# Kernel tuning notes

Hardware: AMD Instinct MI355X
Metric: run time of the kernel (lower is better)

## Reference

```python
import jax, jax.numpy as jnp
import numpy as np

B, C, H, W = 16, 256, 64, 64
WS, NH = 8, 4
HD = C // NH
EPS = 1e-5


def setup_inputs() -> dict:
    key = jax.random.key(0)
    ks = jax.random.split(key, 32)
    s = 0.02
    d = {}
    d['x'] = jax.random.normal(ks[0], (B, C, H, W), jnp.float32)
    d['conv1_w'] = jax.random.normal(ks[1], (C, C, 1, 1), jnp.float32) * s
    d['conv1_b'] = jnp.zeros((C,), jnp.float32)
    d['bn1_g'] = jnp.ones((C,), jnp.float32)
    d['bn1_b'] = jnp.zeros((C,), jnp.float32)
    d['bn1_m'] = jax.random.normal(ks[2], (C,), jnp.float32) * 0.1
    d['bn1_v'] = jax.random.uniform(ks[3], (C,), jnp.float32, 0.5, 1.5)
    d['dw_w'] = jax.random.normal(ks[4], (C, 1, 3, 3), jnp.float32) * s
    d['dw_b'] = jnp.zeros((C,), jnp.float32)
    d['bn2_g'] = jnp.ones((C,), jnp.float32)
    d['bn2_b'] = jnp.zeros((C,), jnp.float32)
    d['bn2_m'] = jax.random.normal(ks[5], (C,), jnp.float32) * 0.1
    d['bn2_v'] = jax.random.uniform(ks[6], (C,), jnp.float32, 0.5, 1.5)
    d['conv3_w'] = jax.random.normal(ks[7], (C, C, 1, 1), jnp.float32) * s
    d['conv3_b'] = jnp.zeros((C,), jnp.float32)
    d['ln1_g'] = jnp.ones((C,), jnp.float32)
    d['ln1_b'] = jnp.zeros((C,), jnp.float32)
    d['qkv_w'] = jax.random.normal(ks[8], (3 * C, C), jnp.float32) * s
    d['qkv_b'] = jnp.zeros((3 * C,), jnp.float32)
    d['proj_w'] = jax.random.normal(ks[9], (C, C), jnp.float32) * s
    d['proj_b'] = jnp.zeros((C,), jnp.float32)
    d['ln2_g'] = jnp.ones((C,), jnp.float32)
    d['ln2_b'] = jnp.zeros((C,), jnp.float32)
    d['mlp_w1'] = jax.random.normal(ks[10], (4 * C, C), jnp.float32) * s
    d['mlp_b1'] = jnp.zeros((4 * C,), jnp.float32)
    d['mlp_w2'] = jax.random.normal(ks[11], (C, 4 * C), jnp.float32) * s
    d['mlp_b2'] = jnp.zeros((C,), jnp.float32)
    return d


def _bn(x, g, b, m, v):
    # eval-mode BatchNorm2d over channel dim of NCHW
    inv = g / jnp.sqrt(v + EPS)
    return x * inv[None, :, None, None] + (b - m * inv)[None, :, None, None]


def _ln(x, g, b):
    mu = x.mean(-1, keepdims=True)
    var = ((x - mu) ** 2).mean(-1, keepdims=True)
    return (x - mu) / jnp.sqrt(var + EPS) * g + b


def reference(x, conv1_w, conv1_b, bn1_g, bn1_b, bn1_m, bn1_v, dw_w, dw_b,
              bn2_g, bn2_b, bn2_m, bn2_v, conv3_w, conv3_b, ln1_g, ln1_b,
              qkv_w, qkv_b, proj_w, proj_b, ln2_g, ln2_b,
              mlp_w1, mlp_b1, mlp_w2, mlp_b2):
    # H,W divisible by WS -> no padding
    # conv path: 1x1 -> BN -> dw3x3 -> BN -> 1x1, residual
    h = jnp.einsum('bchw,oc->bohw', x, conv1_w[:, :, 0, 0]) + conv1_b[None, :, None, None]
    h = _bn(h, bn1_g, bn1_b, bn1_m, bn1_v)
    h = jax.lax.conv_general_dilated(h, dw_w, (1, 1), 'SAME',
                                     feature_group_count=C,
                                     dimension_numbers=('NCHW', 'OIHW', 'NCHW'))
    h = h + dw_b[None, :, None, None]
    h = _bn(h, bn2_g, bn2_b, bn2_m, bn2_v)
    h = jnp.einsum('bchw,oc->bohw', h, conv3_w[:, :, 0, 0]) + conv3_b[None, :, None, None]
    x = x + h

    attn_res = x
    # window partition: (B,C,H,W) -> (B*nWin, WS*WS, C)
    w = x.reshape(B, C, H // WS, WS, W // WS, WS)
    w = w.transpose(0, 2, 4, 3, 5, 1).reshape(-1, WS * WS, C)
    w = _ln(w, ln1_g, ln1_b)

    B_, N, _ = w.shape
    qkv = w @ qkv_w.T + qkv_b                      # (B_, N, 3C)
    qkv = qkv.reshape(B_, N, 3, NH, HD).transpose(2, 0, 3, 1, 4)
    q, k, v = qkv[0], qkv[1], qkv[2]               # (B_, NH, N, HD)
    attn = jax.nn.softmax(jnp.einsum('bhnd,bhmd->bhnm', q, k) * (HD ** -0.5), axis=-1)
    o = jnp.einsum('bhnm,bhmd->bhnd', attn, v)
    o = o.transpose(0, 2, 1, 3).reshape(B_, N, C)
    o = o @ proj_w.T + proj_b
    # window reverse
    o = o.reshape(B, H // WS, W // WS, WS, WS, C)
    o = o.transpose(0, 5, 1, 3, 2, 4).reshape(B, C, H, W)
    x = o + attn_res

    ffn_res = x
    t = x.transpose(0, 2, 3, 1)                    # (B,H,W,C)
    t = _ln(t, ln2_g, ln2_b)
    t = jax.nn.gelu(t @ mlp_w1.T + mlp_b1, approximate=False) @ mlp_w2.T + mlp_b2
    x = ffn_res + t.transpose(0, 3, 1, 2)
    return x
```

## Files before the change

kernel.cpp:

```cpp
#include <hip/hip_runtime.h>
#include <hip/hip_bf16.h>

#define EPS 1e-5f

typedef __attribute__((ext_vector_type(8))) short bf16x8;
typedef __attribute__((ext_vector_type(4))) float f32x4;
typedef __attribute__((ext_vector_type(4))) short s16x4;

__device__ __forceinline__ float b2f(ushort u) {
    union { uint i; float f; } v; v.i = ((uint)u) << 16; return v.f;
}
__device__ __forceinline__ ushort f2b(float f) {
    uint x = __float_as_uint(f);
    return (ushort)((x + 0x7fffu + ((x >> 16) & 1u)) >> 16);
}

#define ASYNC16(dst_lds, src_g) \
    __builtin_amdgcn_global_load_lds((const __attribute__((address_space(1))) void*)(src_g), \
                                     (__attribute__((address_space(3))) void*)(dst_lds), 16, 0, 0)

__global__ void k_fold_conv1(const float* __restrict__ w, const float* __restrict__ cb,
                             const float* __restrict__ g, const float* __restrict__ be,
                             const float* __restrict__ mn, const float* __restrict__ vr,
                             ushort* __restrict__ Wf, float* __restrict__ bf) {
    int i = blockIdx.x * 256 + threadIdx.x;
    int o = i >> 8;
    float inv = g[o] * rsqrtf(vr[o] + EPS);
    Wf[i] = f2b(w[i] * inv);
    if ((i & 255) == 0) bf[o] = cb[o] * inv + be[o] - mn[o] * inv;
}

__global__ void k_fold_dw(const float* __restrict__ w, const float* __restrict__ cb,
                          const float* __restrict__ g, const float* __restrict__ be,
                          const float* __restrict__ mn, const float* __restrict__ vr,
                          float* __restrict__ wT, float* __restrict__ bf) {
    int i = blockIdx.x * 256 + threadIdx.x;
    if (i < 2304) {
        int c = i / 9, k = i % 9;
        float inv = g[c] * rsqrtf(vr[c] + EPS);
        wT[k * 256 + c] = w[i] * inv;
    }
    if (i < 256) {
        float inv = g[i] * rsqrtf(vr[i] + EPS);
        bf[i] = cb[i] * inv + be[i] - mn[i] * inv;
    }
}

__global__ void k_cvt_bf16(const float* __restrict__ s, ushort* __restrict__ d, int n) {
    int i = blockIdx.x * 256 + threadIdx.x;
    if (i < n) d[i] = f2b(s[i]);
}

__global__ __launch_bounds__(256)
void k_transpose_in(const float* __restrict__ x, float* __restrict__ R, ushort* __restrict__ A) {
    __shared__ float T[32][33];
    int b = blockIdx.z;
    int hw0 = blockIdx.x * 32, c0 = blockIdx.y * 32;
    int tx = threadIdx.x & 31, ty = threadIdx.x >> 5;
#pragma unroll
    for (int i = 0; i < 4; ++i) {
        int c = ty + i * 8;
        T[c][tx] = x[((size_t)b * 256 + c0 + c) * 4096 + hw0 + tx];
    }
    __syncthreads();
#pragma unroll
    for (int i = 0; i < 4; ++i) {
        int hwl = ty + i * 8;
        float v = T[tx][hwl];
        size_t t = (size_t)b * 4096 + hw0 + hwl;
        R[t * 256 + c0 + tx] = v;
        A[t * 256 + c0 + tx] = f2b(v);
    }
}

template<int EPI>
__global__ void k_gemm_ws(const ushort* __restrict__ A, const ushort* __restrict__ B,
                          const float* __restrict__ bias,
                          ushort* __restrict__ Co, float* __restrict__ R,
                          int M, int N, int ncol) {
    __shared__ ushort Ws[64 * 256];
    const int tid = threadIdx.x, lane = tid & 63, w = tid >> 6;
    const int lr = lane & 15, lg = lane >> 4;
    const int nwg = gridDim.x, q = nwg >> 3;
    const int wg = (blockIdx.x & 7) * q + (blockIdx.x >> 3);
    const int colb = wg % ncol;
    const int tokt = wg / ncol;
    const int col0 = colb << 6;
    const int tok0 = (tokt << 8) + (w << 6);

#pragma unroll
    for (int i = 0; i < 8; ++i) {
        int g = ((w << 3) + i) << 6;
        int gl = g + lane;
        int feat = gl >> 5, slot = gl & 31;
        ASYNC16(Ws + ((size_t)((w << 3) + i) << 9),
                B + (size_t)(col0 + feat) * 256 + ((slot ^ (feat & 7)) << 3));
    }
    __syncthreads();

    f32x4 acc[4][4];
#pragma unroll
    for (int mf = 0; mf < 4; ++mf)
#pragma unroll
        for (int nf = 0; nf < 4; ++nf) acc[mf][nf] = (f32x4){0.f, 0.f, 0.f, 0.f};

    const int rx7 = lr & 7;
#pragma unroll
    for (int kk = 0; kk < 8; ++kk) {
        bf16x8 a[4], wf[4];
#pragma unroll
        for (int mf = 0; mf < 4; ++mf)
            a[mf] = *(const bf16x8*)(A + (size_t)(tok0 + mf * 16 + lr) * 256 + kk * 32 + lg * 8);
#pragma unroll
        for (int nf = 0; nf < 4; ++nf)
            wf[nf] = *(const bf16x8*)(Ws + (nf * 16 + lr) * 256 + (((kk * 4 + lg) ^ rx7) << 3));
#pragma unroll
        for (int mf = 0; mf < 4; ++mf)
#pragma unroll
            for (int nf = 0; nf < 4; ++nf)
                acc[mf][nf] = __builtin_amdgcn_mfma_f32_16x16x32_bf16(a[mf], wf[nf], acc[mf][nf], 0, 0, 0);
    }

#pragma unroll
    for (int mf = 0; mf < 4; ++mf)
#pragma unroll
        for (int nf = 0; nf < 4; ++nf) {
            int gr0 = tok0 + mf * 16 + lg * 4;
            int gc  = col0 + nf * 16 + lr;
            float bb = bias[gc];
#pragma unroll
            for (int i = 0; i < 4; ++i) {
                float v = acc[mf][nf][i] + bb;
                if (EPI == 0) {
                    Co[(size_t)(gr0 + i) * N + gc] = f2b(v);
                } else if (EPI == 1) {
                    float gl2 = 0.5f * v * (1.0f + erff(v * 0.70710678118f));
                    Co[(size_t)(gr0 + i) * N + gc] = f2b(gl2);
                } else {
                    R[(size_t)(gr0 + i) * 256 + gc] += v;
                }
            }
        }
}

template<int EPI>
__global__ __launch_bounds__(256)
void k_gemm_nt(const ushort* __restrict__ A, const ushort* __restrict__ B,
               const float* __restrict__ bias,
               ushort* __restrict__ Co, float* __restrict__ R, float* __restrict__ Of,
               int M, int N, int K, int ldb) {
    __shared__ ushort As[128 * 64];
    __shared__ ushort Bs[128 * 64];
    int tid = threadIdx.x;
    int lane = tid & 63, w = tid >> 6;
    int row0 = blockIdx.x * 128, col0 = blockIdx.y * 128;
    int wr = (w >> 1) * 64, wc = (w & 1) * 64;
    f32x4 acc[4][4];
#pragma unroll
    for (int mi = 0; mi < 4; ++mi)
#pragma unroll
        for (int ni = 0; ni < 4; ++ni) acc[mi][ni] = (f32x4){0.f, 0.f, 0.f, 0.f};

    int lr = lane & 15, lk = (lane >> 4) << 3;
    int rin = lane >> 3;
    int cin_sw = (((lane & 7) ^ (rin & 7)) << 3);
    int rxor = (lr & 7) << 3;

    for (int k0 = 0; k0 < K; k0 += 64) {
#pragma unroll
        for (int i = 0; i < 4; ++i) {
            int c = (w << 2) + i;
            int r = (c << 3) + rin;
            ASYNC16(As + (c << 9), A + (size_t)(row0 + r) * K + k0 + cin_sw);
            ASYNC16(Bs + (c << 9), B + (size_t)(col0 + r) * ldb + k0 + cin_sw);
        }
        __syncthreads();
#pragma unroll
        for (int kk = 0; kk < 64; kk += 32) {
            bf16x8 af[4], bfm[4];
#pragma unroll
            for (int mi = 0; mi < 4; ++mi)
                af[mi]  = *(const bf16x8*)(As + (wr + mi * 16 + lr) * 64 + ((kk + lk) ^ rxor));
#pragma unroll
            for (int ni = 0; ni < 4; ++ni)
                bfm[ni] = *(const bf16x8*)(Bs + (wc + ni * 16 + lr) * 64 + ((kk + lk) ^ rxor));
#pragma unroll
            for (int mi = 0; mi < 4; ++mi)
#pragma unroll
                for (int ni = 0; ni < 4; ++ni)
                    acc[mi][ni] = __builtin_amdgcn_mfma_f32_16x16x32_bf16(af[mi], bfm[ni], acc[mi][ni], 0, 0, 0);
        }
        __syncthreads();
    }

    int lg = lane >> 4;
#pragma unroll
    for (int mi = 0; mi < 4; ++mi)
#pragma unroll
        for (int ni = 0; ni < 4; ++ni) {
            int gr0 = row0 + wr + mi * 16 + lg * 4;
            int gc  = col0 + wc + ni * 16 + lr;
            int bb = gr0 >> 12, hw0 = gr0 & 4095;
            float* op = Of + ((size_t)(bb * 256 + gc)) * 4096 + hw0;
            f32x4 vv;
            if (EPI == 3) {
                float bbias = bias[gc];
#pragma unroll
                for (int i = 0; i < 4; ++i)
                    vv[i] = acc[mi][ni][i] + bbias + R[(size_t)(gr0 + i) * 256 + gc];
                *(f32x4*)op = vv;
            } else {
                f32x4 old = *(const f32x4*)op;
#pragma unroll
                for (int i = 0; i < 4; ++i) vv[i] = old[i] + acc[mi][ni][i];
                *(f32x4*)op = vv;
            }
        }
}

__global__ __launch_bounds__(256)
void k_dwconv(const ushort* __restrict__ Hin, const float* __restrict__ wT,
              const float* __restrict__ bf, ushort* __restrict__ Out) {
    int tid = threadIdx.x;
    int pg = blockIdx.x * 8 + (tid >> 5);
    int c0 = (tid & 31) << 3;
    int p0 = pg << 2;
    int b12 = p0 & ~4095;
    int hw = p0 & 4095, h0 = hw >> 6, w0 = hw & 63;

    float wreg[9][8];
#pragma unroll
    for (int k = 0; k < 9; ++k) {
        f32x4 a = *(const f32x4*)(wT + k * 256 + c0);
        f32x4 bq = *(const f32x4*)(wT + k * 256 + c0 + 4);
        wreg[k][0] = a.x; wreg[k][1] = a.y; wreg[k][2] = a.z; wreg[k][3] = a.w;
        wreg[k][4] = bq.x; wreg[k][5] = bq.y; wreg[k][6] = bq.z; wreg[k][7] = bq.w;
    }
    float acc[4][8];
    {
        f32x4 b0 = *(const f32x4*)(bf + c0), b1 = *(const f32x4*)(bf + c0 + 4);
#pragma unroll
        for (int px = 0; px < 4; ++px) {
            acc[px][0] = b0.x; acc[px][1] = b0.y; acc[px][2] = b0.z; acc[px][3] = b0.w;
            acc[px][4] = b1.x; acc[px][5] = b1.y; acc[px][6] = b1.z; acc[px][7] = b1.w;
        }
    }
#pragma unroll
    for (int dy = -1; dy <= 1; ++dy) {
        int hy = h0 + dy;
        if ((unsigned)hy >= 64u) continue;
        const ushort* rp = Hin + (((size_t)(b12 + (hy << 6))) << 8) + c0;
#pragma unroll
        for (int dx = -1; dx <= 4; ++dx) {
            int col = w0 + dx;
            if ((unsigned)col >= 64u) continue;
            bf16x8 v = *(const bf16x8*)(rp + ((size_t)col << 8));
            float vf[8];
#pragma unroll
            for (int j = 0; j < 8; ++j) vf[j] = b2f((ushort)v[j]);
#pragma unroll
            for (int px = 0; px < 4; ++px) {
                int kx = dx - px + 1;
                if (kx < 0 || kx > 2) continue;
                int k = (dy + 1) * 3 + kx;
#pragma unroll
                for (int j = 0; j < 8; ++j) acc[px][j] += vf[j] * wreg[k][j];
            }
        }
    }
#pragma unroll
    for (int px = 0; px < 4; ++px) {
        bf16x8 o;
#pragma unroll
        for (int j = 0; j < 8; ++j) o[j] = (short)f2b(acc[px][j]);
        *(bf16x8*)(Out + (size_t)(p0 + px) * 256 + c0) = o;
    }
}

__global__ __launch_bounds__(256)
void k_ln(const float* __restrict__ R, const float* __restrict__ g,
          const float* __restrict__ be, ushort* __restrict__ O) {
    int lane = threadIdx.x & 63;
    size_t t = (size_t)blockIdx.x * 4 + (threadIdx.x >> 6);
    f32x4 v = *(const f32x4*)(R + t * 256 + lane * 4);
    float s = v.x + v.y + v.z + v.w;
    float q = v.x * v.x + v.y * v.y + v.z * v.z + v.w * v.w;
#pragma unroll
    for (int m = 1; m < 64; m <<= 1) { s += __shfl_xor(s, m, 64); q += __shfl_xor(q, m, 64); }
    float mu = s * (1.f / 256.f);
    float rs = rsqrtf(q * (1.f / 256.f) - mu * mu + EPS);
    int c = lane * 4;
    f32x4 gv = *(const f32x4*)(g + c), bv = *(const f32x4*)(be + c);
    s16x4 o;
    o[0] = (short)f2b((v.x - mu) * rs * gv.x + bv.x);
    o[1] = (short)f2b((v.y - mu) * rs * gv.y + bv.y);
    o[2] = (short)f2b((v.z - mu) * rs * gv.z + bv.z);
    o[3] = (short)f2b((v.w - mu) * rs * gv.w + bv.w);
    *(s16x4*)(O + t * 256 + c) = o;
}

__global__ __launch_bounds__(256)
void k_attn(const ushort* __restrict__ QKV, ushort* __restrict__ O) {
    __shared__ ushort SH[4][64 * 68];
    const int tid = threadIdx.x;
    const int w = tid >> 6, lane = tid & 63;
    const int lr = lane & 15, lg = lane >> 4;
    const int win = blockIdx.x;
    const int b = win >> 6, wh = (win >> 3) & 7, ww = win & 7;
    const int rowbase = (b << 12) + (wh << 9) + (ww << 3);
    const int h = w;

#define TROW(tok) (rowbase + (((tok) >> 3) << 6) + ((tok) & 7))

    bf16x8 qB[4][2], kA[4][2], vR[8];
#pragma unroll
    for (int f = 0; f < 4; ++f) {
        size_t t = (size_t)TROW(f * 16 + lr);
        const ushort* qp = QKV + t * 768 + h * 64 + lg * 8;
#pragma unroll
        for (int ks = 0; ks < 2; ++ks) {
            qB[f][ks] = *(const bf16x8*)(qp + ks * 32);
            kA[f][ks] = *(const bf16x8*)(qp + 256 + ks * 32);
        }
    }
    {
        size_t t = (size_t)TROW(lane);
        const ushort* vp = QKV + t * 768 + 512 + h * 64;
#pragma unroll
        for (int i = 0; i < 8; ++i) vR[i] = *(const bf16x8*)(vp + i * 8);
    }

    f32x4 st[4][4];
#pragma unroll
    for (int kf = 0; kf < 4; ++kf)
#pragma unroll
        for (int qf = 0; qf < 4; ++qf) st[kf][qf] = (f32x4){0.f, 0.f, 0.f, 0.f};
#pragma unroll
    for (int ks = 0; ks < 2; ++ks)
#pragma unroll
        for (int kf = 0; kf < 4; ++kf)
#pragma unroll
            for (int qf = 0; qf < 4; ++qf)
                st[kf][qf] = __builtin_amdgcn_mfma_f32_16x16x32_bf16(kA[kf][ks], qB[qf][ks], st[kf][qf], 0, 0, 0);

    ushort* P = &SH[w][0];
#pragma unroll
    for (int qf = 0; qf < 4; ++qf) {
        float m = -1e30f;
#pragma unroll
        for (int kf = 0; kf < 4; ++kf)
#pragma unroll
            for (int i = 0; i < 4; ++i) m = fmaxf(m, st[kf][qf][i]);
        m = fmaxf(m, __shfl_xor(m, 16, 64));
        m = fmaxf(m, __shfl_xor(m, 32, 64));
        m *= 0.125f;
        float sum = 0.f;
#pragma unroll
        for (int kf = 0; kf < 4; ++kf) {
            f32x4 e;
#pragma unroll
            for (int i = 0; i < 4; ++i) { e[i] = __expf(st[kf][qf][i] * 0.125f - m); sum += e[i]; }
            st[kf][qf] = e;
        }
        sum += __shfl_xor(sum, 16, 64);
        sum += __shfl_xor(sum, 32, 64);
        float rl = 1.f / sum;
#pragma unroll
        for (int kf = 0; kf < 4; ++kf) {
            s16x4 pk;
#pragma unroll
            for (int i = 0; i < 4; ++i) pk[i] = (short)f2b(st[kf][qf][i] * rl);
            *(s16x4*)(P + (qf * 16 + lr) * 68 + kf * 16 + lg * 4) = pk;
        }
    }
    bf16x8 pA[4][2];
#pragma unroll
    for (int mf = 0; mf < 4; ++mf)
#pragma unroll
        for (int ks = 0; ks < 2; ++ks) {
            union { bf16x8 v8; s16x4 v4[2]; } u;
            const ushort* p = P + (mf * 16 + lr) * 68 + ks * 32 + lg * 8;
            u.v4[0] = *(const s16x4*)(p);
            u.v4[1] = *(const s16x4*)(p + 4);
            pA[mf][ks] = u.v8;
        }
    asm volatile("s_waitcnt lgkmcnt(0)" ::: "memory");
    __builtin_amdgcn_sched_barrier(0);
#pragma unroll
    for (int i = 0; i < 8; ++i) {
        union { bf16x8 v8; s16x4 v4[2]; } u; u.v8 = vR[i];
        *(s16x4*)(P + lane * 68 + i * 8) = u.v4[0];
        *(s16x4*)(P + lane * 68 + i * 8 + 4) = u.v4[1];
    }
    asm volatile("s_waitcnt lgkmcnt(0)" ::: "memory");
    __builtin_amdgcn_sched_barrier(0);
    bf16x8 vB[4][2];
#pragma unroll
    for (int nf = 0; nf < 4; ++nf)
#pragma unroll
        for (int ks = 0; ks < 2; ++ks) {
            bf16x8 vb;
#pragma unroll
            for (int j = 0; j < 8; ++j)
                vb[j] = (short)P[(ks * 32 + lg * 8 + j) * 68 + nf * 16 + lr];
            vB[nf][ks] = vb;
        }
    f32x4 o[4][4];
#pragma unroll
    for (int mf = 0; mf < 4; ++mf)
#pragma unroll
        for (int nf = 0; nf < 4; ++nf) o[mf][nf] = (f32x4){0.f, 0.f, 0.f, 0.f};
#pragma unroll
    for (int ks = 0; ks < 2; ++ks)
#pragma unroll
        for (int mf = 0; mf < 4; ++mf)
#pragma unroll
            for (int nf = 0; nf < 4; ++nf)
                o[mf][nf] = __builtin_amdgcn_mfma_f32_16x16x32_bf16(pA[mf][ks], vB[nf][ks], o[mf][nf], 0, 0, 0);
#pragma unroll
    for (int mf = 0; mf < 4; ++mf)
#pragma unroll
        for (int nf = 0; nf < 4; ++nf)
#pragma unroll
            for (int i = 0; i < 4; ++i) {
                int q = mf * 16 + lg * 4 + i;
                int d = nf * 16 + lr;
                O[(size_t)TROW(q) * 256 + h * 64 + d] = f2b(o[mf][nf][i]);
            }
#undef TROW
}

extern "C" void kernel_launch(void* const* d_in, const int* in_sizes, int n_in,
                              void* d_out, int out_size, void* d_ws, size_t ws_size,
                              hipStream_t stream) {
    const float* x       = (const float*)d_in[0];
    const float* conv1_w = (const float*)d_in[1];
    const float* conv1_b = (const float*)d_in[2];
    const float* bn1_g   = (const float*)d_in[3];
    const float* bn1_b   = (const float*)d_in[4];
    const float* bn1_m   = (const float*)d_in[5];
    const float* bn1_v   = (const float*)d_in[6];
    const float* dw_w    = (const float*)d_in[7];
    const float* dw_b    = (const float*)d_in[8];
    const float* bn2_g   = (const float*)d_in[9];
    const float* bn2_b   = (const float*)d_in[10];
    const float* bn2_m   = (const float*)d_in[11];
    const float* bn2_v   = (const float*)d_in[12];
    const float* conv3_w = (const float*)d_in[13];
    const float* conv3_b = (const float*)d_in[14];
    const float* ln1_g   = (const float*)d_in[15];
    const float* ln1_b   = (const float*)d_in[16];
    const float* qkv_w   = (const float*)d_in[17];
    const float* qkv_b   = (const float*)d_in[18];
    const float* proj_w  = (const float*)d_in[19];
    const float* proj_b  = (const float*)d_in[20];
    const float* ln2_g   = (const float*)d_in[21];
    const float* ln2_b   = (const float*)d_in[22];
    const float* mlp_w1  = (const float*)d_in[23];
    const float* mlp_b1  = (const float*)d_in[24];
    const float* mlp_w2  = (const float*)d_in[25];
    const float* mlp_b2  = (const float*)d_in[26];
    float* out = (float*)d_out;

    char* ws = (char*)d_ws;
    float*  R    = (float*)(ws);
    ushort* Abuf = (ushort*)(ws + (64u  << 20));
    ushort* H1   = (ushort*)(ws + (96u  << 20));
    ushort* BIG  = (ushort*)(ws + (128u << 20));
    char* wp = ws + (224u << 20);
    ushort* W1f  = (ushort*)wp; wp += 131072;
    float*  b1f  = (float*)wp;  wp += 1024;
    float*  wdwT = (float*)wp;  wp += 9216;
    float*  bdw  = (float*)wp;  wp += 1024;
    ushort* W3   = (ushort*)wp; wp += 131072;
    ushort* Wqkv = (ushort*)wp; wp += 393216;
    ushort* Wproj= (ushort*)wp; wp += 131072;
    ushort* Wm1  = (ushort*)wp; wp += 524288;
    ushort* Wm2  = (ushort*)wp; wp += 524288;

    k_fold_conv1<<<256, 256, 0, stream>>>(conv1_w, conv1_b, bn1_g, bn1_b, bn1_m, bn1_v, W1f, b1f);
    k_fold_dw<<<9, 256, 0, stream>>>(dw_w, dw_b, bn2_g, bn2_b, bn2_m, bn2_v, wdwT, bdw);
    k_cvt_bf16<<<256, 256, 0, stream>>>(conv3_w, W3, 65536);
    k_cvt_bf16<<<768, 256, 0, stream>>>(qkv_w, Wqkv, 196608);
    k_cvt_bf16<<<256, 256, 0, stream>>>(proj_w, Wproj, 65536);
    k_cvt_bf16<<<1024, 256, 0, stream>>>(mlp_w1, Wm1, 262144);
    k_cvt_bf16<<<1024, 256, 0, stream>>>(mlp_w2, Wm2, 262144);

    k_transpose_in<<<dim3(128, 8, 16), 256, 0, stream>>>(x, R, Abuf);

    k_gemm_ws<0><<<1024, 256, 0, stream>>>(Abuf, W1f, b1f, H1, nullptr, 65536, 256, 4);
    k_dwconv<<<2048, 256, 0, stream>>>(H1, wdwT, bdw, Abuf);
    k_gemm_ws<2><<<1024, 256, 0, stream>>>(Abuf, W3, conv3_b, nullptr, R, 65536, 256, 4);

    k_ln<<<16384, 256, 0, stream>>>(R, ln1_g, ln1_b, Abuf);
    k_gemm_ws<0><<<3072, 256, 0, stream>>>(Abuf, Wqkv, qkv_b, BIG, nullptr, 65536, 768, 12);
    k_attn<<<1024, 256, 0, stream>>>(BIG, H1);
    k_gemm_ws<2><<<1024, 256, 0, stream>>>(H1, Wproj, proj_b, nullptr, R, 65536, 256, 4);

    k_ln<<<16384, 256, 0, stream>>>(R, ln2_g, ln2_b, Abuf);
    k_gemm_ws<1><<<2048, 256, 0, stream>>>(Abuf, Wm1, mlp_b1, BIG, nullptr, 65536, 512, 8);
    k_gemm_nt<3><<<dim3(512, 2), 256, 0, stream>>>(BIG, Wm2, mlp_b2, nullptr, R, out, 65536, 256, 512, 1024);
    k_gemm_ws<1><<<2048, 256, 0, stream>>>(Abuf, Wm1 + 512 * 256, mlp_b1 + 512, BIG, nullptr, 65536, 512, 8);
    k_gemm_nt<4><<<dim3(512, 2), 256, 0, stream>>>(BIG, Wm2 + 512, nullptr, nullptr, nullptr, out, 65536, 256, 512, 1024);
}
```

Before: 503.5 us.

## Widen weight-stationary GEMM tile to 128 columns and double-buffer A fragments

The weight-stationary GEMM now stages 128 output columns of weights in LDS (64 KB) instead of 64, so each wave computes a 64x128 tile and every A fragment loaded from global memory is reused across twice as many MFMAs. A fragments are software-pipelined with two register buffers, prefetching the next k-slice while the current one is computed, and the first A load overlaps the async LDS weight fill. Grid sizes are halved to match. The cost is more accumulator registers (128 floats per lane) and more LDS per block, which lowers occupancy, and fewer blocks are launched.

```diff
diff --git a/kernel.cpp b/kernel.cpp
--- a/kernel.cpp
+++ b/kernel.cpp
@@ -78,53 +78,75 @@
                           const float* __restrict__ bias,
                           ushort* __restrict__ Co, float* __restrict__ R,
                           int M, int N, int ncol) {
-    __shared__ ushort Ws[64 * 256];
+    __shared__ ushort Ws[128 * 256];
     const int tid = threadIdx.x, lane = tid & 63, w = tid >> 6;
     const int lr = lane & 15, lg = lane >> 4;
     const int nwg = gridDim.x, q = nwg >> 3;
     const int wg = (blockIdx.x & 7) * q + (blockIdx.x >> 3);
     const int colb = wg % ncol;
     const int tokt = wg / ncol;
-    const int col0 = colb << 6;
+    const int col0 = colb << 7;
     const int tok0 = (tokt << 8) + (w << 6);
 
 #pragma unroll
-    for (int i = 0; i < 8; ++i) {
-        int g = ((w << 3) + i) << 6;
-        int gl = g + lane;
+    for (int i = 0; i < 16; ++i) {
+        int c = (w << 4) + i;
+        int gl = (c << 6) + lane;
         int feat = gl >> 5, slot = gl & 31;
-        ASYNC16(Ws + ((size_t)((w << 3) + i) << 9),
+        ASYNC16(Ws + ((size_t)c << 9),
                 B + (size_t)(col0 + feat) * 256 + ((slot ^ (feat & 7)) << 3));
     }
+
+    const ushort* ap = A + (size_t)tok0 * 256 + lg * 8;
+#define LOADA(dst, kk)                                                                     \
+    _Pragma("unroll")                                                                      \
+    for (int mf = 0; mf < 4; ++mf)                                                         \
+        dst[mf] = *(const bf16x8*)(ap + (size_t)(mf * 16 + lr) * 256 + (kk) * 32);
+
+    bf16x8 aX[4], aY[4];
+    LOADA(aX, 0)
     __syncthreads();
 
-    f32x4 acc[4][4];
+    f32x4 acc[4][8];
 #pragma unroll
     for (int mf = 0; mf < 4; ++mf)
 #pragma unroll
-        for (int nf = 0; nf < 4; ++nf) acc[mf][nf] = (f32x4){0.f, 0.f, 0.f, 0.f};
+        for (int nf = 0; nf < 8; ++nf) acc[mf][nf] = (f32x4){0.f, 0.f, 0.f, 0.f};
 
     const int rx7 = lr & 7;
 #pragma unroll
-    for (int kk = 0; kk < 8; ++kk) {
-        bf16x8 a[4], wf[4];
-#pragma unroll
-        for (int mf = 0; mf < 4; ++mf)
-            a[mf] = *(const bf16x8*)(A + (size_t)(tok0 + mf * 16 + lr) * 256 + kk * 32 + lg * 8);
-#pragma unroll
-        for (int nf = 0; nf < 4; ++nf)
-            wf[nf] = *(const bf16x8*)(Ws + (nf * 16 + lr) * 256 + (((kk * 4 + lg) ^ rx7) << 3));
-#pragma unroll
-        for (int mf = 0; mf < 4; ++mf)
-#pragma unroll
-            for (int nf = 0; nf < 4; ++nf)
-                acc[mf][nf] = __builtin_amdgcn_mfma_f32_16x16x32_bf16(a[mf], wf[nf], acc[mf][nf], 0, 0, 0);
-    }
+    for (int kk = 0; kk < 8; kk += 2) {
+        LOADA(aY, kk + 1)
+        {
+            bf16x8 wf[8];
+#pragma unroll
+            for (int nf = 0; nf < 8; ++nf)
+                wf[nf] = *(const bf16x8*)(Ws + (nf * 16 + lr) * 256 + (((kk * 4 + lg) ^ rx7) << 3));
+#pragma unroll
+            for (int mf = 0; mf < 4; ++mf)
+#pragma unroll
+                for (int nf = 0; nf < 8; ++nf)
+                    acc[mf][nf] = __builtin_amdgcn_mfma_f32_16x16x32_bf16(aX[mf], wf[nf], acc[mf][nf], 0, 0, 0);
+        }
+        if (kk + 2 < 8) { LOADA(aX, kk + 2) }
+        {
+            bf16x8 wf[8];
+#pragma unroll
+            for (int nf = 0; nf < 8; ++nf)
+                wf[nf] = *(const bf16x8*)(Ws + (nf * 16 + lr) * 256 + ((((kk + 1) * 4 + lg) ^ rx7) << 3));
+#pragma unroll
+            for (int mf = 0; mf < 4; ++mf)
+#pragma unroll
+                for (int nf = 0; nf < 8; ++nf)
+                    acc[mf][nf] = __builtin_amdgcn_mfma_f32_16x16x32_bf16(aY[mf], wf[nf], acc[mf][nf], 0, 0, 0);
+        }
+    }
+#undef LOADA
 
 #pragma unroll
     for (int mf = 0; mf < 4; ++mf)
 #pragma unroll
-        for (int nf = 0; nf < 4; ++nf) {
+        for (int nf = 0; nf < 8; ++nf) {
             int gr0 = tok0 + mf * 16 + lg * 4;
             int gc  = col0 + nf * 16 + lr;
             float bb = bias[gc];
@@ -488,18 +510,18 @@
 
     k_transpose_in<<<dim3(128, 8, 16), 256, 0, stream>>>(x, R, Abuf);
 
-    k_gemm_ws<0><<<1024, 256, 0, stream>>>(Abuf, W1f, b1f, H1, nullptr, 65536, 256, 4);
+    k_gemm_ws<0><<<512, 256, 0, stream>>>(Abuf, W1f, b1f, H1, nullptr, 65536, 256, 2);
     k_dwconv<<<2048, 256, 0, stream>>>(H1, wdwT, bdw, Abuf);
-    k_gemm_ws<2><<<1024, 256, 0, stream>>>(Abuf, W3, conv3_b, nullptr, R, 65536, 256, 4);
+    k_gemm_ws<2><<<512, 256, 0, stream>>>(Abuf, W3, conv3_b, nullptr, R, 65536, 256, 2);
 
     k_ln<<<16384, 256, 0, stream>>>(R, ln1_g, ln1_b, Abuf);
-    k_gemm_ws<0><<<3072, 256, 0, stream>>>(Abuf, Wqkv, qkv_b, BIG, nullptr, 65536, 768, 12);
+    k_gemm_ws<0><<<1536, 256, 0, stream>>>(Abuf, Wqkv, qkv_b, BIG, nullptr, 65536, 768, 6);
     k_attn<<<1024, 256, 0, stream>>>(BIG, H1);
-    k_gemm_ws<2><<<1024, 256, 0, stream>>>(H1, Wproj, proj_b, nullptr, R, 65536, 256, 4);
+    k_gemm_ws<2><<<512, 256, 0, stream>>>(H1, Wproj, proj_b, nullptr, R, 65536, 256, 2);
 
     k_ln<<<16384, 256, 0, stream>>>(R, ln2_g, ln2_b, Abuf);
-    k_gemm_ws<1><<<2048, 256, 0, stream>>>(Abuf, Wm1, mlp_b1, BIG, nullptr, 65536, 512, 8);
+    k_gemm_ws<1><<<1024, 256, 0, stream>>>(Abuf, Wm1, mlp_b1, BIG, nullptr, 65536, 512, 4);
     k_gemm_nt<3><<<dim3(512, 2), 256, 0, stream>>>(BIG, Wm2, mlp_b2, nullptr, R, out, 65536, 256, 512, 1024);
-    k_gemm_ws<1><<<2048, 256, 0, stream>>>(Abuf, Wm1 + 512 * 256, mlp_b1 + 512, BIG, nullptr, 65536, 512, 8);
+    k_gemm_ws<1><<<1024, 256, 0, stream>>>(Abuf, Wm1 + 512 * 256, mlp_b1 + 512, BIG, nullptr, 65536, 512, 4);
     k_gemm_nt<4><<<dim3(512, 2), 256, 0, stream>>>(BIG, Wm2 + 512, nullptr, nullptr, nullptr, out, 65536, 256, 512, 1024);
 }
```

Result: slower. 1.456 ms (+189.2%).
